# Performance work log

Hardware: AMD Instinct MI355X
Metric: run time of the kernel (lower is better)

The kernel has to match this reference:

```python
import jax, jax.numpy as jnp
import numpy as np
from jax import lax

B, V_ECC, V_ERR, T, C = 8192, 16, 12, 25, 32
F_IN = C * T           # 800 = temporal_out * tf_num
G = 64                 # gcn_out
H2 = 256               # hidden_size * 2
EHR_DIM, EHR_OUT = 64, 64

def _lhat(V):
    # bidirectional ring graph; PyG ChebConv sym-norm with lambda_max=2.0:
    # L_hat = (2/lmax) * (I - D^-1/2 A D^-1/2) - I = -D^-1/2 A D^-1/2
    i = np.arange(V)
    src = np.concatenate([i, (i + 1) % V])
    dst = np.concatenate([(i + 1) % V, i])
    A = np.zeros((V, V), np.float32)
    A[src, dst] = 1.0
    deg = A.sum(1)
    dinv = np.where(deg > 0, deg ** -0.5, 0.0).astype(np.float32)
    return jnp.asarray(-(dinv[:, None] * A * dinv[None, :]))

LHAT_ECC = _lhat(V_ECC)
LHAT_ERR = _lhat(V_ERR)

def setup_inputs():
    key = jax.random.key(0)
    ks = jax.random.split(key, 23)
    n = lambda k, s: jax.random.normal(k, s, jnp.float32) * 0.02
    return {
        "ecc": jax.random.normal(ks[0], (B, V_ECC, T), jnp.float32),
        "err": jax.random.normal(ks[1], (B, V_ERR, T), jnp.float32),
        "ehr": jax.random.normal(ks[2], (B, EHR_DIM), jnp.float32),
        "wt_ecc": n(ks[3], (C, 1, 3)), "bt_ecc": n(ks[4], (C,)),
        "wt_err": n(ks[5], (C, 1, 3)), "bt_err": n(ks[6], (C,)),
        "W0_ecc": n(ks[7], (F_IN, G)), "W1_ecc": n(ks[8], (F_IN, G)), "b_ecc": n(ks[9], (G,)),
        "W0_err": n(ks[10], (F_IN, G)), "W1_err": n(ks[11], (F_IN, G)), "b_err": n(ks[12], (G,)),
        "Wp_ecc": n(ks[13], (V_ECC * G, H2)), "bp_ecc": n(ks[14], (H2,)),
        "Wp_err": n(ks[15], (V_ERR * G, H2)), "bp_err": n(ks[16], (H2,)),
        "Wa": n(ks[17], (H2, 1)), "ba": n(ks[18], (1,)),
        "We": n(ks[19], (EHR_DIM, EHR_OUT)), "be": n(ks[20], (EHR_OUT,)),
        "Wf2": n(ks[21], (H2 + EHR_OUT, 1)), "bf2": n(ks[22], (1,)),
    }

def _temporal(x, w, b):
    # x: [B, V, T]; Conv1d(1 -> C, k=3, padding=1) per node, then flatten (C, T)
    bb, v, t = x.shape
    y = lax.conv_general_dilated(x.reshape(bb * v, 1, t), w, (1,), "SAME",
                                 dimension_numbers=("NCH", "OIH", "NCH"))
    y = y + b[None, :, None]
    return y.reshape(bb, v, -1)        # [B, V, C*T]

def _cheb(x, lhat, w0, w1, b):
    # K=2 ChebConv: out = T0(x)@W0 + T1(x)@W1 + b, T1 = L_hat x (batched over B)
    tx1 = jnp.einsum("uv,bvd->bud", lhat, x)
    return x @ w0 + tx1 @ w1 + b

def reference(ecc, err, ehr, wt_ecc, bt_ecc, wt_err, bt_err,
              W0_ecc, W1_ecc, b_ecc, W0_err, W1_err, b_err,
              Wp_ecc, bp_ecc, Wp_err, bp_err, Wa, ba, We, be, Wf2, bf2):
    bsz = ecc.shape[0]
    ecc_f = _temporal(ecc, wt_ecc, bt_ecc)                    # [B,16,800]
    err_f = _temporal(err, wt_err, bt_err)                    # [B,12,800]
    ecc_out = _cheb(ecc_f, LHAT_ECC, W0_ecc, W1_ecc, b_ecc)   # [B,16,64]
    err_out = _cheb(err_f, LHAT_ERR, W0_err, W1_err, b_err)   # [B,12,64]
    ecc_g = ecc_out.reshape(bsz, -1) @ Wp_ecc + bp_ecc        # [B,256]
    err_g = err_out.reshape(bsz, -1) @ Wp_err + bp_err        # [B,256]
    attn = jax.nn.sigmoid(jnp.tanh(ecc_g + err_g) @ Wa + ba)  # [B,1]
    fused = attn * ecc_g + (1.0 - attn) * err_g
    ehr_p = jax.nn.relu(ehr @ We + be)                        # dropout = identity (eval)
    combined = jnp.concatenate([fused, ehr_p], axis=1)        # [B,320]
    x = jax.nn.relu(combined)
    return jax.nn.sigmoid(x @ Wf2 + bf2)                      # [B,1]
```

## Files before the change

### kernel.cpp

```cpp
#include <hip/hip_runtime.h>
#include <math.h>

#define B_TOT 8192
#define KE 400
#define KR 300
#define MEP 416
#define MRP 320
#define ROWS 16

#define SXE_LD 424
#define SXR_LD 328
#define SEH_LD 72

#define OFF_WEFF0E 0
#define OFF_WEFF1E 1600
#define OFF_WEFF0R 3200
#define OFF_WEFF1R 4800
#define OFF_CVE    6400
#define OFF_CVR    6464
#define OFF_BE     6528
#define OFF_BR     6784
#define U_AET 14080
#define U_ART (U_AET + 256 * MEP)
#define U_WET (U_ART + 256 * MRP)

typedef __attribute__((ext_vector_type(8))) short short8;
typedef __attribute__((ext_vector_type(4))) float floatx4;

__device__ __forceinline__ float sigmoidf_(float x) { return 1.f / (1.f + __expf(-x)); }
__device__ __forceinline__ float tanhf_(float x) { float e = __expf(2.f * x); return (e - 1.f) / (e + 1.f); }
__device__ __forceinline__ unsigned short f2bf(float x) {
    unsigned u = __float_as_uint(x);
    u += 0x7fffu + ((u >> 16) & 1u);
    return (unsigned short)(u >> 16);
}

__global__ __launch_bounds__(256) void fold_temporal(
    const float* __restrict__ wt_ecc, const float* __restrict__ bt_ecc,
    const float* __restrict__ wt_err, const float* __restrict__ bt_err,
    const float* __restrict__ W0_ecc, const float* __restrict__ W1_ecc, const float* __restrict__ b_ecc,
    const float* __restrict__ W0_err, const float* __restrict__ W1_err, const float* __restrict__ b_err,
    float* __restrict__ ws)
{
    const int blk = blockIdx.x;
    const int tid = threadIdx.x;
    const int cq = tid >> 6;
    const int g  = tid & 63;

    __shared__ float red[4][64];

    if (blk < 100) {
        const int m = blk / 25;
        const int tin = blk % 25;
        const bool is_err = (m >= 2);
        const float* wt = is_err ? wt_err : wt_ecc;
        const float* W = (m & 1) ? (is_err ? W1_err : W1_ecc) : (is_err ? W0_err : W0_ecc);
        const int t0 = tin > 0 ? tin - 1 : 0;
        const int t1 = tin < 24 ? tin + 1 : 24;
        float s = 0.f;
        #pragma unroll
        for (int c8 = 0; c8 < 8; ++c8) {
            const int c = cq * 8 + c8;
            for (int t = t0; t <= t1; ++t) {
                const int k = tin - t + 1;
                s = fmaf(wt[c * 3 + k], W[(c * 25 + t) * 64 + g], s);
            }
        }
        red[cq][g] = s;
        __syncthreads();
        if (tid < 64)
            ws[m * 1600 + tin * 64 + g] = red[0][g] + red[1][g] + red[2][g] + red[3][g];
    } else if (blk < 102) {
        const bool is_err = (blk == 101);
        const float* bt = is_err ? bt_err : bt_ecc;
        const float* W0 = is_err ? W0_err : W0_ecc;
        const float* W1 = is_err ? W1_err : W1_ecc;
        const float* bb = is_err ? b_err : b_ecc;
        float s = 0.f;
        #pragma unroll
        for (int c8 = 0; c8 < 8; ++c8) {
            const int c = cq * 8 + c8;
            const float btc = bt[c];
            #pragma unroll
            for (int t = 0; t < 25; ++t) {
                const int ct = (c * 25 + t) * 64 + g;
                s = fmaf(btc, W0[ct] - W1[ct], s);
            }
        }
        red[cq][g] = s;
        __syncthreads();
        if (tid < 64)
            ws[(is_err ? OFF_CVR : OFF_CVE) + g] =
                bb[g] + red[0][g] + red[1][g] + red[2][g] + red[3][g];
    } else {
        ws[OFF_BE + tid] = 0.f;
        ws[OFF_BR + tid] = 0.f;
    }
}

__global__ __launch_bounds__(256) void fold_graph(
    const float* __restrict__ Wp_ecc, const float* __restrict__ bp_ecc,
    const float* __restrict__ Wp_err, const float* __restrict__ bp_err,
    const float* __restrict__ We,
    float* __restrict__ wsf, unsigned short* __restrict__ wsu)
{
    const int blk = blockIdx.x;
    const int h = threadIdx.x;

    if (blk < MEP) {
        const int k = blk;
        float s = 0.f;
        if (k < KE) {
            const int v = k / 25, tin = k % 25;
            const int vp = (v + 1) & 15, vm = (v + 15) & 15;
            const float* w0 = wsf + OFF_WEFF0E + tin * 64;
        const float* w1 = wsf + OFF_WEFF1E + tin * 64;
            #pragma unroll 4
            for (int g = 0; g < 64; ++g) {
                s = fmaf(w0[g], Wp_ecc[(v * 64 + g) * 256 + h], s);
                s = fmaf(-0.5f * w1[g], Wp_ecc[(vp * 64 + g) * 256 + h] + Wp_ecc[(vm * 64 + g) * 256 + h], s);
            }
        }
        wsu[U_AET + (size_t)h * MEP + k] = f2bf(s);
    } else if (blk < MEP + MRP) {
        const int k = blk - MEP;
        float s = 0.f;
        if (k < KR) {
            const int v = k / 25, tin = k % 25;
            const int vp = (v + 1) % 12, vm = (v + 11) % 12;
            const float* w0 = wsf + OFF_WEFF0R + tin * 64;
            const float* w1 = wsf + OFF_WEFF1R + tin * 64;
            #pragma unroll 4
            for (int g = 0; g < 64; ++g) {
                s = fmaf(w0[g], Wp_err[(v * 64 + g) * 256 + h], s);
                s = fmaf(-0.5f * w1[g], Wp_err[(vp * 64 + g) * 256 + h] + Wp_err[(vm * 64 + g) * 256 + h], s);
            }
        }
        wsu[U_ART + (size_t)h * MRP + k] = f2bf(s);
    } else if (blk < MEP + MRP + 16) {
        const int i = blk - (MEP + MRP);
        const float* cv = wsf + OFF_CVE;
        float s = (i == 0) ? bp_ecc[h] : 0.f;
        #pragma unroll 4
        for (int jj = 0; jj < 64; ++jj) {
            const int j = i * 64 + jj;
            s = fmaf(cv[j & 63], Wp_ecc[(size_t)j * 256 + h], s);
        }
        atomicAdd(&wsf[OFF_BE + h], s);
    } else if (blk < MEP + MRP + 32) {
        const int i = blk - (MEP + MRP + 16);
        const float* cv = wsf + OFF_CVR;
        float s = (i == 0) ? bp_err[h] : 0.f;
        if (i < 12) {
            #pragma unroll 4
            for (int jj = 0; jj < 64; ++jj) {
                const int j = i * 64 + jj;
                s = fmaf(cv[j & 63], Wp_err[(size_t)j * 256 + h], s);
            }
        }
        atomicAdd(&wsf[OFF_BR + h], s);
    } else {
        for (int it = 0; it < 16; ++it) {
            const int idx = it * 256 + h;
            const int e = idx >> 6, d = idx & 63;
            wsu[U_WET + e * 64 + d] = f2bf(We[d * 64 + e]);
        }
    }
}

__global__ __launch_bounds__(256, 4) void fused_main(
    const float* __restrict__ ecc, const float* __restrict__ err, const float* __restrict__ ehr,
    const float* __restrict__ wsf, const unsigned short* __restrict__ wsu,
    const float* __restrict__ Wa, const float* __restrict__ ba,
    const float* __restrict__ be_, const float* __restrict__ Wf2, const float* __restrict__ bf2,
    float* __restrict__ out)
{
    const unsigned short* awt_e = wsu + U_AET;
    const unsigned short* awt_r = wsu + U_ART;
    const unsigned short* wet   = wsu + U_WET;
    const float* biasE = wsf + OFF_BE;
    const float* biasR = wsf + OFF_BR;

    __shared__ __align__(16) char smem[ROWS * (SXE_LD + SXR_LD + SEH_LD) * 2];
    unsigned short* sxe = (unsigned short*)smem;
    unsigned short* sxr = sxe + ROWS * SXE_LD;
    unsigned short* seh = sxr + ROWS * SXR_LD;
    float* pa_part = (float*)smem;
    float* at_arr  = pa_part + 64;
    float* po_part = at_arr + 16;

    const int tid = threadIdx.x;
    const int row0 = blockIdx.x * ROWS;

    for (int it = 0; it < 7; ++it) {
        const int f = it * 256 + tid;
        if (f < ROWS * 106) {
            const int r = f / 106, q = f - r * 106;
            float4 v = make_float4(0.f, 0.f, 0.f, 0.f);
            if (q < 100) v = *(const float4*)(ecc + (size_t)(row0 + r) * KE + q * 4);
            const unsigned p0 = (unsigned)f2bf(v.x) | ((unsigned)f2bf(v.y) << 16);
            const unsigned p1 = (unsigned)f2bf(v.z) | ((unsigned)f2bf(v.w) << 16);
            *(uint2*)&sxe[r * SXE_LD + q * 4] = make_uint2(p0, p1);
        }
    }
    for (int it = 0; it < 6; ++it) {
        const int f = it * 256 + tid;
        if (f < ROWS * 82) {
            const int r = f / 82, q = f - r * 82;
            float4 v = make_float4(0.f, 0.f, 0.f, 0.f);
            if (q < 75) v = *(const float4*)(err + (size_t)(row0 + r) * KR + q * 4);
            const unsigned p0 = (unsigned)f2bf(v.x) | ((unsigned)f2bf(v.y) << 16);
            const unsigned p1 = (unsigned)f2bf(v.z) | ((unsigned)f2bf(v.w) << 16);
            *(uint2*)&sxr[r * SXR_LD + q * 4] = make_uint2(p0, p1);
        }
    }
    {
        const int r = tid >> 4, q = tid & 15;
        const float4 v = *(const float4*)(ehr + (size_t)(row0 + r) * 64 + q * 4);
        const unsigned p0 = (unsigned)f2bf(v.x) | ((unsigned)f2bf(v.y) << 16);
        const unsigned p1 = (unsigned)f2bf(v.z) | ((unsigned)f2bf(v.w) << 16);
        *(uint2*)&seh[r * SEH_LD + q * 4] = make_uint2(p0, p1);
    }
    __syncthreads();

    const int wv = tid >> 6, lane = tid & 63;
    const int lm = lane & 15, lq = lane >> 4;
    const int n0 = wv * 64;

    floatx4 accE[4], accR[4], accH;
    accH = (floatx4){0.f, 0.f, 0.f, 0.f};
    #pragma unroll
    for (int nt = 0; nt < 4; ++nt) {
        accE[nt] = (floatx4){0.f, 0.f, 0.f, 0.f};
        accR[nt] = (floatx4){0.f, 0.f, 0.f, 0.f};
    }

    #pragma unroll
    for (int kc = 0; kc < 2; ++kc) {
        const short8 b = *(const short8*)(wet + (wv * 16 + lm) * 64 + kc * 32 + lq * 8);
        const short8 a = *(const short8*)&seh[lm * SEH_LD + kc * 32 + lq * 8];
        accH = __builtin_amdgcn_mfma_f32_16x16x32_bf16(a, b, accH, 0, 0, 0);
    }
    #pragma unroll
    for (int kc = 0; kc < 13; ++kc) {
        const short8 a0 = *(const short8*)&sxe[lm * SXE_LD + kc * 32 + lq * 8];
        #pragma unroll
        for (int nt = 0; nt < 4; ++nt) {
            const short8 b = *(const short8*)(awt_e + (size_t)(n0 + nt * 16 + lm) * MEP + kc * 32 + lq * 8);
            accE[nt] = __builtin_amdgcn_mfma_f32_16x16x32_bf16(a0, b, accE[nt], 0, 0, 0);
        }
    }
    #pragma unroll
    for (int kc = 0; kc < 10; ++kc) {
        const short8 a0 = *(const short8*)&sxr[lm * SXR_LD + kc * 32 + lq * 8];
        #pragma unroll
        for (int nt = 0; nt < 4; ++nt) {
            const short8 b = *(const short8*)(awt_r + (size_t)(n0 + nt * 16 + lm) * MRP + kc * 32 + lq * 8);
            accR[nt] = __builtin_amdgcn_mfma_f32_16x16x32_bf16(a0, b, accR[nt], 0, 0, 0);
        }
    }

    float bE[4], bR[4], wa[4], wf[4];
    #pragma unroll
    for (int nt = 0; nt < 4; ++nt) {
        const int h = n0 + nt * 16 + lm;
        bE[nt] = biasE[h]; bR[nt] = biasR[h]; wa[nt] = Wa[h]; wf[nt] = Wf2[h];
    }
    const int e_lane = wv * 16 + lm;
    const float eh_be = be_[e_lane];
    const float eh_wf = Wf2[256 + e_lane];

    float pa_lane[4];
    #pragma unroll
    for (int rg = 0; rg < 4; ++rg) {
        float s = 0.f;
        #pragma unroll
        for (int nt = 0; nt < 4; ++nt) {
            const float ev = accE[nt][rg] + bE[nt];
            const float rv = accR[nt][rg] + bR[nt];
            s = fmaf(tanhf_(ev + rv), wa[nt], s);
        }
        s += __shfl_xor(s, 1, 64); s += __shfl_xor(s, 2, 64);
        s += __shfl_xor(s, 4, 64); s += __shfl_xor(s, 8, 64);
        pa_lane[rg] = s;
    }

    __syncthreads();
    if (lm == 0) {
        #pragma unroll
        for (int rg = 0; rg < 4; ++rg)
            pa_part[wv * 16 + lq * 4 + rg] = pa_lane[rg];
    }
    __syncthreads();
    if (tid < 16)
        at_arr[tid] = sigmoidf_(pa_part[tid] + pa_part[16 + tid] + pa_part[32 + tid] + pa_part[48 + tid] + ba[0]);
    __syncthreads();

    float po_lane[4];
    #pragma unroll
    for (int rg = 0; rg < 4; ++rg) {
        const int r = lq * 4 + rg;
        const float at = at_arr[r];
        const float om = 1.f - at;
        float s = 0.f;
        #pragma unroll
        for (int nt = 0; nt < 4; ++nt) {
            const float ev = accE[nt][rg] + bE[nt];
            const float rv = accR[nt][rg] + bR[nt];
            s = fmaf(fmaxf(at * ev + om * rv, 0.f), wf[nt], s);
        }
        s = fmaf(fmaxf(accH[rg] + eh_be, 0.f), eh_wf, s);
        s += __shfl_xor(s, 1, 64); s += __shfl_xor(s, 2, 64);
        s += __shfl_xor(s, 4, 64); s += __shfl_xor(s, 8, 64);
        po_lane[rg] = s;
    }
    if (lm == 0) {
        #pragma unroll
        for (int rg = 0; rg < 4; ++rg)
            po_part[wv * 16 + lq * 4 + rg] = po_lane[rg];
    }
    __syncthreads();
    if (tid < 16)
        out[row0 + tid] = sigmoidf_(po_part[tid] + po_part[16 + tid] + po_part[32 + tid] + po_part[48 + tid] + bf2[0]);
}

extern "C" void kernel_launch(void* const* d_in, const int* in_sizes, int n_in,
                              void* d_out, int out_size, void* d_ws, size_t ws_size,
                              hipStream_t stream)
{
    (void)in_sizes; (void)n_in; (void)out_size; (void)ws_size;
    const float* ecc    = (const float*)d_in[0];
    const float* err    = (const float*)d_in[1];
    const float* ehr    = (const float*)d_in[2];
    const float* wt_ecc = (const float*)d_in[3];
    const float* bt_ecc = (const float*)d_in[4];
    const float* wt_err = (const float*)d_in[5];
    const float* bt_err = (const float*)d_in[6];
    const float* W0_ecc = (const float*)d_in[7];
    const float* W1_ecc = (const float*)d_in[8];
    const float* b_ecc  = (const float*)d_in[9];
    const float* W0_err = (const float*)d_in[10];
    const float* W1_err = (const float*)d_in[11];
    const float* b_err  = (const float*)d_in[12];
    const float* Wp_ecc = (const float*)d_in[13];
    const float* bp_ecc = (const float*)d_in[14];
    const float* Wp_err = (const float*)d_in[15];
    const float* bp_err = (const float*)d_in[16];
    const float* Wa     = (const float*)d_in[17];
    const float* ba     = (const float*)d_in[18];
    const float* We     = (const float*)d_in[19];
    const float* be     = (const float*)d_in[20];
    const float* Wf2    = (const float*)d_in[21];
    const float* bf2    = (const float*)d_in[22];
    float* wsf = (float*)d_ws;
    unsigned short* wsu = (unsigned short*)d_ws;
    float* out = (float*)d_out;

    fold_temporal<<<dim3(103), dim3(256), 0, stream>>>(
        wt_ecc, bt_ecc, wt_err, bt_err, W0_ecc, W1_ecc, b_ecc, W0_err, W1_err, b_err, wsf);
    fold_graph<<<dim3(MEP + MRP + 32 + 1), dim3(256), 0, stream>>>(
        Wp_ecc, bp_ecc, Wp_err, bp_err, We, wsf, wsu);
    fused_main<<<dim3(B_TOT / ROWS), dim3(256), 0, stream>>>(
        ecc, err, ehr, wsf, wsu, Wa, ba, be, Wf2, bf2, out);
}
```

Measured before the change: 150.9 us.

## Merge temporal and graph weight-folding kernels into one launch

Combines the two weight-folding kernels into a single kernel. Each block now recomputes the temporal-conv-folded Cheb weights it needs in shared memory before projecting through Wp, rather than reading them from a buffer filled by a previous launch. The bias folding now writes per-chunk partial sums that fused_main adds together, which removes the atomics and the zero-init pass. This saves one launch and its serialization, at the price of redundant recomputation of the temporal fold in each block.

```diff
diff --git a/kernel.cpp b/kernel.cpp
--- a/kernel.cpp
+++ b/kernel.cpp
@@ -12,14 +12,8 @@
 #define SXR_LD 328
 #define SEH_LD 72
 
-#define OFF_WEFF0E 0
-#define OFF_WEFF1E 1600
-#define OFF_WEFF0R 3200
-#define OFF_WEFF1R 4800
-#define OFF_CVE    6400
-#define OFF_CVR    6464
-#define OFF_BE     6528
-#define OFF_BR     6784
+#define OFF_BE 0
+#define OFF_BR 1024
 #define U_AET 14080
 #define U_ART (U_AET + 256 * MEP)
 #define U_WET (U_ART + 256 * MRP)
@@ -35,49 +29,77 @@
     return (unsigned short)(u >> 16);
 }
 
-__global__ __launch_bounds__(256) void fold_temporal(
+__global__ __launch_bounds__(256) void fold_all(
     const float* __restrict__ wt_ecc, const float* __restrict__ bt_ecc,
     const float* __restrict__ wt_err, const float* __restrict__ bt_err,
     const float* __restrict__ W0_ecc, const float* __restrict__ W1_ecc, const float* __restrict__ b_ecc,
     const float* __restrict__ W0_err, const float* __restrict__ W1_err, const float* __restrict__ b_err,
-    float* __restrict__ ws)
+    const float* __restrict__ Wp_ecc, const float* __restrict__ bp_ecc,
+    const float* __restrict__ Wp_err, const float* __restrict__ bp_err,
+    const float* __restrict__ We,
+    float* __restrict__ wsf, unsigned short* __restrict__ wsu)
 {
     const int blk = blockIdx.x;
     const int tid = threadIdx.x;
-    const int cq = tid >> 6;
-    const int g  = tid & 63;
-
     __shared__ float red[4][64];
-
-    if (blk < 100) {
-        const int m = blk / 25;
-        const int tin = blk % 25;
-        const bool is_err = (m >= 2);
+    __shared__ float comb[2][64];
+
+    if (blk < MEP + MRP) {
+        const bool is_err = blk >= MEP;
+        const int k  = is_err ? blk - MEP : blk;
+        const int K  = is_err ? KR : KE;
+        const int MP = is_err ? MRP : MEP;
+        unsigned short* dst = wsu + (is_err ? U_ART : U_AET);
+        if (k >= K) { dst[(size_t)tid * MP + k] = 0; return; }
+
+        const int v = k / 25, tin = k % 25;
+        const int V = is_err ? 12 : 16;
+        const int vp = (v + 1) % V, vm = (v + V - 1) % V;
         const float* wt = is_err ? wt_err : wt_ecc;
-        const float* W = (m & 1) ? (is_err ? W1_err : W1_ecc) : (is_err ? W0_err : W0_ecc);
+        const float* W0 = is_err ? W0_err : W0_ecc;
+        const float* W1 = is_err ? W1_err : W1_ecc;
+        const float* Wp = is_err ? Wp_err : Wp_ecc;
+
+        const int part = tid >> 6, g = tid & 63;
+        const float* W = (part >> 1) ? W1 : W0;
+        const int c0 = (part & 1) * 16;
         const int t0 = tin > 0 ? tin - 1 : 0;
         const int t1 = tin < 24 ? tin + 1 : 24;
         float s = 0.f;
-        #pragma unroll
-        for (int c8 = 0; c8 < 8; ++c8) {
-            const int c = cq * 8 + c8;
-            for (int t = t0; t <= t1; ++t) {
-                const int k = tin - t + 1;
-                s = fmaf(wt[c * 3 + k], W[(c * 25 + t) * 64 + g], s);
-            }
-        }
-        red[cq][g] = s;
+        for (int ci = 0; ci < 16; ++ci) {
+            const int c = c0 + ci;
+            for (int t = t0; t <= t1; ++t)
+                s = fmaf(wt[c * 3 + (tin - t + 1)], W[(c * 25 + t) * 64 + g], s);
+        }
+        red[part][g] = s;
         __syncthreads();
-        if (tid < 64)
-            ws[m * 1600 + tin * 64 + g] = red[0][g] + red[1][g] + red[2][g] + red[3][g];
-    } else if (blk < 102) {
-        const bool is_err = (blk == 101);
+        if (tid < 128) {
+            const int o = tid >> 6;
+            comb[o][g] = red[o * 2 + 0][g] + red[o * 2 + 1][g];
+        }
+        __syncthreads();
+
+        const int h = tid;
+        float acc = 0.f;
+        #pragma unroll 4
+        for (int g2 = 0; g2 < 64; ++g2) {
+            acc = fmaf(comb[0][g2], Wp[(v * 64 + g2) * 256 + h], acc);
+            acc = fmaf(-0.5f * comb[1][g2], Wp[(vp * 64 + g2) * 256 + h] + Wp[(vm * 64 + g2) * 256 + h], acc);
+        }
+        dst[(size_t)h * MP + k] = f2bf(acc);
+    } else if (blk < MEP + MRP + 7) {
+        const int bi = blk - (MEP + MRP);
+        const bool is_err = bi >= 4;
+        const int i = is_err ? bi - 4 : bi;
         const float* bt = is_err ? bt_err : bt_ecc;
         const float* W0 = is_err ? W0_err : W0_ecc;
         const float* W1 = is_err ? W1_err : W1_ecc;
         const float* bb = is_err ? b_err : b_ecc;
+        const float* Wp = is_err ? Wp_err : Wp_ecc;
+        const float* bp = is_err ? bp_err : bp_ecc;
+
+        const int g = tid & 63, cq = tid >> 6;
         float s = 0.f;
-        #pragma unroll
         for (int c8 = 0; c8 < 8; ++c8) {
             const int c = cq * 8 + c8;
             const float btc = bt[c];
@@ -90,78 +112,20 @@
         red[cq][g] = s;
         __syncthreads();
         if (tid < 64)
-            ws[(is_err ? OFF_CVR : OFF_CVE) + g] =
-                bb[g] + red[0][g] + red[1][g] + red[2][g] + red[3][g];
-    } else {
-        ws[OFF_BE + tid] = 0.f;
-        ws[OFF_BR + tid] = 0.f;
-    }
-}
-
-__global__ __launch_bounds__(256) void fold_graph(
-    const float* __restrict__ Wp_ecc, const float* __restrict__ bp_ecc,
-    const float* __restrict__ Wp_err, const float* __restrict__ bp_err,
-    const float* __restrict__ We,
-    float* __restrict__ wsf, unsigned short* __restrict__ wsu)
-{
-    const int blk = blockIdx.x;
-    const int h = threadIdx.x;
-
-    if (blk < MEP) {
-        const int k = blk;
-        float s = 0.f;
-        if (k < KE) {
-            const int v = k / 25, tin = k % 25;
-            const int vp = (v + 1) & 15, vm = (v + 15) & 15;
-            const float* w0 = wsf + OFF_WEFF0E + tin * 64;
-        const float* w1 = wsf + OFF_WEFF1E + tin * 64;
-            #pragma unroll 4
-            for (int g = 0; g < 64; ++g) {
-                s = fmaf(w0[g], Wp_ecc[(v * 64 + g) * 256 + h], s);
-                s = fmaf(-0.5f * w1[g], Wp_ecc[(vp * 64 + g) * 256 + h] + Wp_ecc[(vm * 64 + g) * 256 + h], s);
-            }
-        }
-        wsu[U_AET + (size_t)h * MEP + k] = f2bf(s);
-    } else if (blk < MEP + MRP) {
-        const int k = blk - MEP;
-        float s = 0.f;
-        if (k < KR) {
-            const int v = k / 25, tin = k % 25;
-            const int vp = (v + 1) % 12, vm = (v + 11) % 12;
-            const float* w0 = wsf + OFF_WEFF0R + tin * 64;
-            const float* w1 = wsf + OFF_WEFF1R + tin * 64;
-            #pragma unroll 4
-            for (int g = 0; g < 64; ++g) {
-                s = fmaf(w0[g], Wp_err[(v * 64 + g) * 256 + h], s);
-                s = fmaf(-0.5f * w1[g], Wp_err[(vp * 64 + g) * 256 + h] + Wp_err[(vm * 64 + g) * 256 + h], s);
-            }
-        }
-        wsu[U_ART + (size_t)h * MRP + k] = f2bf(s);
-    } else if (blk < MEP + MRP + 16) {
-        const int i = blk - (MEP + MRP);
-        const float* cv = wsf + OFF_CVE;
-        float s = (i == 0) ? bp_ecc[h] : 0.f;
+            comb[0][g] = bb[g] + red[0][g] + red[1][g] + red[2][g] + red[3][g];
+        __syncthreads();
+
+        const int h = tid;
+        float acc = (i == 0) ? bp[h] : 0.f;
         #pragma unroll 4
-        for (int jj = 0; jj < 64; ++jj) {
-            const int j = i * 64 + jj;
-            s = fmaf(cv[j & 63], Wp_ecc[(size_t)j * 256 + h], s);
-        }
-        atomicAdd(&wsf[OFF_BE + h], s);
-    } else if (blk < MEP + MRP + 32) {
-        const int i = blk - (MEP + MRP + 16);
-        const float* cv = wsf + OFF_CVR;
-        float s = (i == 0) ? bp_err[h] : 0.f;
-        if (i < 12) {
-            #pragma unroll 4
-            for (int jj = 0; jj < 64; ++jj) {
-                const int j = i * 64 + jj;
-                s = fmaf(cv[j & 63], Wp_err[(size_t)j * 256 + h], s);
-            }
-        }
-        atomicAdd(&wsf[OFF_BR + h], s);
+        for (int jj = 0; jj < 256; ++jj) {
+            const int j = i * 256 + jj;
+            acc = fmaf(comb[0][j & 63], Wp[(size_t)j * 256 + h], acc);
+        }
+        wsf[(is_err ? OFF_BR : OFF_BE) + i * 256 + h] = acc;
     } else {
         for (int it = 0; it < 16; ++it) {
-            const int idx = it * 256 + h;
+            const int idx = it * 256 + tid;
             const int e = idx >> 6, d = idx & 63;
             wsu[U_WET + e * 64 + d] = f2bf(We[d * 64 + e]);
         }
@@ -264,7 +228,9 @@
     #pragma unroll
     for (int nt = 0; nt < 4; ++nt) {
         const int h = n0 + nt * 16 + lm;
-        bE[nt] = biasE[h]; bR[nt] = biasR[h]; wa[nt] = Wa[h]; wf[nt] = Wf2[h];
+        bE[nt] = biasE[h] + biasE[256 + h] + biasE[512 + h] + biasE[768 + h];
+        bR[nt] = biasR[h] + biasR[256 + h] + biasR[512 + h];
+        wa[nt] = Wa[h]; wf[nt] = Wf2[h];
     }
     const int e_lane = wv * 16 + lm;
     const float eh_be = be_[e_lane];
@@ -356,9 +322,8 @@
     unsigned short* wsu = (unsigned short*)d_ws;
     float* out = (float*)d_out;
 
-    fold_temporal<<<dim3(103), dim3(256), 0, stream>>>(
-        wt_ecc, bt_ecc, wt_err, bt_err, W0_ecc, W1_ecc, b_ecc, W0_err, W1_err, b_err, wsf);
-    fold_graph<<<dim3(MEP + MRP + 32 + 1), dim3(256), 0, stream>>>(
+    fold_all<<<dim3(MEP + MRP + 7 + 1), dim3(256), 0, stream>>>(
+        wt_ecc, bt_ecc, wt_err, bt_err, W0_ecc, W1_ecc, b_ecc, W0_err, W1_err, b_err,
         Wp_ecc, bp_ecc, Wp_err, bp_err, We, wsf, wsu);
     fused_main<<<dim3(B_TOT / ROWS), dim3(256), 0, stream>>>(
         ecc, err, ehr, wsf, wsu, Wa, ba, be, Wf2, bf2, out);
```

Measured after the change: 170.1 us. 1.13x slower.

## Restructure graph weight fold to reuse Wp loads across time steps, drop atomics

Applied to the files above, without the earlier changes.

The fold_graph kernel now uses one block per graph node instead of one block per (node, time) output column. Each Wp element is loaded once and reused across all 25 time steps through register accumulators, with the temporal weights staged transposed in shared memory. The bias reduction writes per-block partial sums that fused_main adds up, so the atomics and the zero-init block in fold_temporal are gone. The grid shrinks from about 769 blocks to 44, which cuts redundant global reads of Wp but leaves less parallelism and adds a few bias loads per thread in the main kernel.

```diff
diff --git a/kernel.cpp b/kernel.cpp
--- a/kernel.cpp
+++ b/kernel.cpp
@@ -19,8 +19,8 @@
 #define OFF_CVE    6400
 #define OFF_CVR    6464
 #define OFF_BE     6528
-#define OFF_BR     6784
-#define U_AET 14080
+#define OFF_BR     8576
+#define U_AET 20480
 #define U_ART (U_AET + 256 * MEP)
 #define U_WET (U_ART + 256 * MRP)
 
@@ -70,7 +70,7 @@
         __syncthreads();
         if (tid < 64)
             ws[m * 1600 + tin * 64 + g] = red[0][g] + red[1][g] + red[2][g] + red[3][g];
-    } else if (blk < 102) {
+    } else {
         const bool is_err = (blk == 101);
         const float* bt = is_err ? bt_err : bt_ecc;
         const float* W0 = is_err ? W0_err : W0_ecc;
@@ -92,9 +92,6 @@
         if (tid < 64)
             ws[(is_err ? OFF_CVR : OFF_CVE) + g] =
                 bb[g] + red[0][g] + red[1][g] + red[2][g] + red[3][g];
-    } else {
-        ws[OFF_BE + tid] = 0.f;
-        ws[OFF_BR + tid] = 0.f;
     }
 }
 
@@ -105,63 +102,90 @@
     float* __restrict__ wsf, unsigned short* __restrict__ wsu)
 {
     const int blk = blockIdx.x;
-    const int h = threadIdx.x;
-
-    if (blk < MEP) {
-        const int k = blk;
-        float s = 0.f;
-        if (k < KE) {
-            const int v = k / 25, tin = k % 25;
-            const int vp = (v + 1) & 15, vm = (v + 15) & 15;
-            const float* w0 = wsf + OFF_WEFF0E + tin * 64;
-        const float* w1 = wsf + OFF_WEFF1E + tin * 64;
-            #pragma unroll 4
-            for (int g = 0; g < 64; ++g) {
-                s = fmaf(w0[g], Wp_ecc[(v * 64 + g) * 256 + h], s);
-                s = fmaf(-0.5f * w1[g], Wp_ecc[(vp * 64 + g) * 256 + h] + Wp_ecc[(vm * 64 + g) * 256 + h], s);
+    const int tid = threadIdx.x;
+
+    if (blk < 28) {
+        const bool is_err = blk >= 16;
+        const int v  = is_err ? blk - 16 : blk;
+        const int V  = is_err ? 12 : 16;
+        const int MP = is_err ? MRP : MEP;
+        const float* Wp = is_err ? Wp_err : Wp_ecc;
+        const float* wsrc0 = wsf + (is_err ? OFF_WEFF0R : OFF_WEFF0E);
+        const float* wsrc1 = wsf + (is_err ? OFF_WEFF1R : OFF_WEFF1E);
+        unsigned short* dst = wsu + (is_err ? U_ART : U_AET);
+        const int vp = (v + 1) % V, vm = (v + V - 1) % V;
+
+        __shared__ __align__(16) float w0T[64][28];
+        __shared__ __align__(16) float w1T[64][28];
+        for (int i = tid; i < 64 * 28; i += 256) {
+            ((float*)w0T)[i] = 0.f; ((float*)w1T)[i] = 0.f;
+        }
+        __syncthreads();
+        for (int i = tid; i < 1600; i += 256) {
+            const int tin = i >> 6, g = i & 63;
+            w0T[g][tin] = wsrc0[i];
+            w1T[g][tin] = -0.5f * wsrc1[i];
+        }
+        __syncthreads();
+
+        const int h = tid;
+        float acc[25];
+        #pragma unroll
+        for (int t = 0; t < 25; ++t) acc[t] = 0.f;
+
+        #pragma unroll 2
+        for (int g = 0; g < 64; ++g) {
+            const float p0 = Wp[(size_t)(v  * 64 + g) * 256 + h];
+            const float ps = Wp[(size_t)(vm * 64 + g) * 256 + h]
+                           + Wp[(size_t)(vp * 64 + g) * 256 + h];
+            #pragma unroll
+            for (int tc = 0; tc < 6; ++tc) {
+                const float4 a = *(const float4*)&w0T[g][tc * 4];
+                const float4 b = *(const float4*)&w1T[g][tc * 4];
+                acc[tc * 4 + 0] = fmaf(a.x, p0, fmaf(b.x, ps, acc[tc * 4 + 0]));
+                acc[tc * 4 + 1] = fmaf(a.y, p0, fmaf(b.y, ps, acc[tc * 4 + 1]));
+                acc[tc * 4 + 2] = fmaf(a.z, p0, fmaf(b.z, ps, acc[tc * 4 + 2]));
+                acc[tc * 4 + 3] = fmaf(a.w, p0, fmaf(b.w, ps, acc[tc * 4 + 3]));
             }
-        }
-        wsu[U_AET + (size_t)h * MEP + k] = f2bf(s);
-    } else if (blk < MEP + MRP) {
-        const int k = blk - MEP;
-        float s = 0.f;
-        if (k < KR) {
-            const int v = k / 25, tin = k % 25;
-            const int vp = (v + 1) % 12, vm = (v + 11) % 12;
-            const float* w0 = wsf + OFF_WEFF0R + tin * 64;
-            const float* w1 = wsf + OFF_WEFF1R + tin * 64;
-            #pragma unroll 4
-            for (int g = 0; g < 64; ++g) {
-                s = fmaf(w0[g], Wp_err[(v * 64 + g) * 256 + h], s);
-                s = fmaf(-0.5f * w1[g], Wp_err[(vp * 64 + g) * 256 + h] + Wp_err[(vm * 64 + g) * 256 + h], s);
-            }
-        }
-        wsu[U_ART + (size_t)h * MRP + k] = f2bf(s);
-    } else if (blk < MEP + MRP + 16) {
-        const int i = blk - (MEP + MRP);
+            acc[24] = fmaf(w0T[g][24], p0, fmaf(w1T[g][24], ps, acc[24]));
+        }
+        #pragma unroll
+        for (int t = 0; t < 25; ++t)
+            dst[(size_t)h * MP + v * 25 + t] = f2bf(acc[t]);
+    } else if (blk == 28) {
+        for (int i = tid; i < 256 * 16; i += 256) {
+            const int h = i >> 4, k = 400 + (i & 15);
+            wsu[U_AET + (size_t)h * MEP + k] = 0;
+        }
+        for (int i = tid; i < 256 * 20; i += 256) {
+            const int h = i / 20, k = 300 + (i % 20);
+            wsu[U_ART + (size_t)h * MRP + k] = 0;
+        }
+    } else if (blk < 29 + 8) {
+        const int i = blk - 29;
         const float* cv = wsf + OFF_CVE;
-        float s = (i == 0) ? bp_ecc[h] : 0.f;
+        const int h = tid;
+        float acc = (i == 0) ? bp_ecc[h] : 0.f;
         #pragma unroll 4
-        for (int jj = 0; jj < 64; ++jj) {
-            const int j = i * 64 + jj;
-            s = fmaf(cv[j & 63], Wp_ecc[(size_t)j * 256 + h], s);
-        }
-        atomicAdd(&wsf[OFF_BE + h], s);
-    } else if (blk < MEP + MRP + 32) {
-        const int i = blk - (MEP + MRP + 16);
+        for (int jj = 0; jj < 128; ++jj) {
+            const int j = i * 128 + jj;
+            acc = fmaf(cv[j & 63], Wp_ecc[(size_t)j * 256 + h], acc);
+        }
+        wsf[OFF_BE + i * 256 + h] = acc;
+    } else if (blk < 37 + 6) {
+        const int i = blk - 37;
         const float* cv = wsf + OFF_CVR;
-        float s = (i == 0) ? bp_err[h] : 0.f;
-        if (i < 12) {
-            #pragma unroll 4
-            for (int jj = 0; jj < 64; ++jj) {
-                const int j = i * 64 + jj;
-                s = fmaf(cv[j & 63], Wp_err[(size_t)j * 256 + h], s);
-            }
-        }
-        atomicAdd(&wsf[OFF_BR + h], s);
+        const int h = tid;
+        float acc = (i == 0) ? bp_err[h] : 0.f;
+        #pragma unroll 4
+        for (int jj = 0; jj < 128; ++jj) {
+            const int j = i * 128 + jj;
+            acc = fmaf(cv[j & 63], Wp_err[(size_t)j * 256 + h], acc);
+        }
+        wsf[OFF_BR + i * 256 + h] = acc;
     } else {
         for (int it = 0; it < 16; ++it) {
-            const int idx = it * 256 + h;
+            const int idx = it * 256 + tid;
             const int e = idx >> 6, d = idx & 63;
             wsu[U_WET + e * 64 + d] = f2bf(We[d * 64 + e]);
         }
@@ -264,7 +288,14 @@
     #pragma unroll
     for (int nt = 0; nt < 4; ++nt) {
         const int h = n0 + nt * 16 + lm;
-        bE[nt] = biasE[h]; bR[nt] = biasR[h]; wa[nt] = Wa[h]; wf[nt] = Wf2[h];
+        float se = 0.f;
+        #pragma unroll
+        for (int p = 0; p < 8; ++p) se += biasE[p * 256 + h];
+        float sr = 0.f;
+        #pragma unroll
+        for (int p = 0; p < 6; ++p) sr += biasR[p * 256 + h];
+        bE[nt] = se; bR[nt] = sr;
+        wa[nt] = Wa[h]; wf[nt] = Wf2[h];
     }
     const int e_lane = wv * 16 + lm;
     const float eh_be = be_[e_lane];
@@ -356,9 +387,9 @@
     unsigned short* wsu = (unsigned short*)d_ws;
     float* out = (float*)d_out;
 
-    fold_temporal<<<dim3(103), dim3(256), 0, stream>>>(
+    fold_temporal<<<dim3(102), dim3(256), 0, stream>>>(
         wt_ecc, bt_ecc, wt_err, bt_err, W0_ecc, W1_ecc, b_ecc, W0_err, W1_err, b_err, wsf);
-    fold_graph<<<dim3(MEP + MRP + 32 + 1), dim3(256), 0, stream>>>(
+    fold_graph<<<dim3(44), dim3(256), 0, stream>>>(
         Wp_ecc, bp_ecc, Wp_err, bp_err, We, wsf, wsu);
     fused_main<<<dim3(B_TOT / ROWS), dim3(256), 0, stream>>>(
         ecc, err, ehr, wsf, wsu, Wa, ba, be, Wf2, bf2, out);
```

New measurement: 159.1 us. 5.4% more time.
